# Kernel optimization log

Hardware: AMD Instinct MI355X
Metric: run time of the kernel (lower is better)

The kernel has to match this reference:

```python
import jax, jax.numpy as jnp
import numpy as np

NUM_HEADS = 4
GROUPS = 16
EPS = 1e-5


def setup_inputs() -> dict:
    key = jax.random.key(0)
    ks = jax.random.split(key, 7)
    b, c, hh, ww = 4, 256, 64, 64
    x = jax.random.normal(ks[0], (b, c, hh, ww), dtype=jnp.float32)
    norm_w = 1.0 + 0.1 * jax.random.normal(ks[1], (c,), dtype=jnp.float32)
    norm_b = 0.1 * jax.random.normal(ks[2], (c,), dtype=jnp.float32)
    qkv_w = jax.random.normal(ks[3], (3 * c, c), dtype=jnp.float32) / np.sqrt(c)
    qkv_b = 0.01 * jax.random.normal(ks[4], (3 * c,), dtype=jnp.float32)
    # NOTE: original zero-inits proj_out; we use random weights so the
    # attention path actually affects the output (kernel correctness test).
    proj_w = jax.random.normal(ks[5], (c, c), dtype=jnp.float32) / np.sqrt(c)
    proj_b = jnp.zeros((c,), dtype=jnp.float32)
    return {"x": x, "norm_w": norm_w, "norm_b": norm_b,
            "qkv_w": qkv_w, "qkv_b": qkv_b,
            "proj_w": proj_w, "proj_b": proj_b}


def _group_norm(x, w, b):
    # x: [B, C, T]; GroupNorm32 computes in fp32 (inputs already fp32)
    B, C, T = x.shape
    xg = x.reshape(B, GROUPS, C // GROUPS, T)
    mean = jnp.mean(xg, axis=(2, 3), keepdims=True)
    var = jnp.var(xg, axis=(2, 3), keepdims=True)
    xn = ((xg - mean) * jax.lax.rsqrt(var + EPS)).reshape(B, C, T)
    return xn * w[None, :, None] + b[None, :, None]


def reference(x, norm_w, norm_b, qkv_w, qkv_b, proj_w, proj_b):
    b, c = x.shape[0], x.shape[1]
    spatial = x.shape[2:]
    x2 = x.reshape(b, c, -1)                       # [B, C, T]
    T = x2.shape[-1]
    normed = _group_norm(x2, norm_w, norm_b)
    qkv = jnp.einsum('oc,bct->bot', qkv_w, normed) + qkv_b[None, :, None]
    # faithful reshape: [B, 3C, T] -> [B*H, 3C/H, T], then split in thirds
    qkv = qkv.reshape(b * NUM_HEADS, (3 * c) // NUM_HEADS, T)
    ch = qkv.shape[1] // 3                         # = C / H
    q, k, v = jnp.split(qkv, 3, axis=1)
    scale = 1.0 / np.sqrt(np.sqrt(ch))
    weight = jnp.einsum('bct,bcs->bts', q * scale, k * scale)
    weight = jax.nn.softmax(weight.astype(jnp.float32), axis=-1).astype(qkv.dtype)
    h = jnp.einsum('bts,bcs->bct', weight, v)      # [B*H, ch, T]
    h = h.reshape(b, c, T)
    h = jnp.einsum('oc,bct->bot', proj_w, h) + proj_b[None, :, None]
    return (x2 + h).reshape(b, c, *spatial)
```

## Files before the change

### kernel.cpp

```cpp
#include <hip/hip_runtime.h>

constexpr int kB  = 4;
constexpr int kC  = 256;
constexpr int kT  = 4096;
constexpr int kG  = 16;
constexpr int kCg = kC / kG;
constexpr int kH  = 4;
constexpr int kCh = kC / kH;
constexpr float kEps = 1e-5f;
constexpr float kQScale = 0.125f * 1.4426950408889634f;

typedef short bf16x8 __attribute__((ext_vector_type(8)));
typedef float f32x4  __attribute__((ext_vector_type(4)));
typedef float f32x16 __attribute__((ext_vector_type(16)));

__device__ inline unsigned short f2bf(float f) {
    union { float f; unsigned u; } v; v.f = f;
    unsigned r = v.u + 0x7fffu + ((v.u >> 16) & 1u);
    return (unsigned short)(r >> 16);
}
__device__ inline unsigned pk2bf(float a, float b) {
    return (unsigned)f2bf(a) | ((unsigned)f2bf(b) << 16);
}
__device__ inline unsigned pk2bf_trunc(float a, float b) {
    return __builtin_amdgcn_perm(__float_as_uint(b), __float_as_uint(a), 0x07060302u);
}

__global__ __launch_bounds__(256) void gn_stats_kernel(const float* __restrict__ x,
                                                       float* __restrict__ stats) {
    int bg = blockIdx.x;
    const float4* xp4 = (const float4*)(x + (size_t)bg * (kCg * kT));
    int tid = threadIdx.x;
    float s = 0.f, q = 0.f;
    #pragma unroll 4
    for (int i = 0; i < (kCg * kT / 4) / 256; ++i) {
        float4 v = xp4[tid + i * 256];
        s += v.x + v.y + v.z + v.w;
        q += v.x * v.x + v.y * v.y + v.z * v.z + v.w * v.w;
    }
    #pragma unroll
    for (int off = 32; off > 0; off >>= 1) {
        s += __shfl_down(s, off);
        q += __shfl_down(q, off);
    }
    __shared__ float rs[4], rq[4];
    int wid = tid >> 6, lane = tid & 63;
    if (lane == 0) { rs[wid] = s; rq[wid] = q; }
    __syncthreads();
    if (tid == 0) {
        float S = rs[0] + rs[1] + rs[2] + rs[3];
        float Q = rq[0] + rq[1] + rq[2] + rq[3];
        const float invN = 1.0f / (float)(kCg * kT);
        float mean = S * invN;
        float var  = Q * invN - mean * mean;
        stats[bg * 2 + 0] = mean;
        stats[bg * 2 + 1] = rsqrtf(var + kEps);
    }
}

__global__ __launch_bounds__(256) void gn_apply_t_kernel(const float* __restrict__ x,
                                                         const float* __restrict__ stats,
                                                         const float* __restrict__ w,
                                                         const float* __restrict__ bias,
                                                         unsigned short* __restrict__ normT) {
    __shared__ float Ls[64][65];
    int t0 = blockIdx.x * 64;
    int c0 = blockIdx.y * 64;
    int b  = blockIdx.z;
    int tid = threadIdx.x;
    #pragma unroll
    for (int p = 0; p < 4; ++p) {
        int idx = tid + p * 256;
        int cl = idx >> 4, t4 = idx & 15;
        int c = c0 + cl;
        int bg = b * kG + (c >> 4);
        float mean = stats[bg * 2 + 0];
        float rstd = stats[bg * 2 + 1];
        float sw = w[c] * rstd;
        float sb = bias[c] - mean * sw;
        float4 v = *(const float4*)&x[((size_t)b * kC + c) * kT + t0 + t4 * 4];
        Ls[t4 * 4 + 0][cl] = v.x * sw + sb;
        Ls[t4 * 4 + 1][cl] = v.y * sw + sb;
        Ls[t4 * 4 + 2][cl] = v.z * sw + sb;
        Ls[t4 * 4 + 3][cl] = v.w * sw + sb;
    }
    __syncthreads();
    {
        int row = tid >> 2, cq = (tid & 3) * 16;
        unsigned tmp[8];
        #pragma unroll
        for (int i = 0; i < 8; ++i)
            tmp[i] = pk2bf(Ls[row][cq + 2 * i], Ls[row][cq + 2 * i + 1]);
        uint4* dst = (uint4*)&normT[((size_t)b * kT + t0 + row) * kC + c0 + cq];
        dst[0] = make_uint4(tmp[0], tmp[1], tmp[2], tmp[3]);
        dst[1] = make_uint4(tmp[4], tmp[5], tmp[6], tmp[7]);
    }
}

__global__ __launch_bounds__(256) void wcvt_kernel(const float* __restrict__ qkv_w,
                                                   const float* __restrict__ proj_w,
                                                   unsigned short* __restrict__ wbf) {
    int gid = blockIdx.x * 256 + threadIdx.x;
    for (int i = gid; i < 65536; i += gridDim.x * 256) {
        float4 v = (i < 49152) ? ((const float4*)qkv_w)[i]
                               : ((const float4*)proj_w)[i - 49152];
        *(uint2*)&wbf[(size_t)i * 4] = make_uint2(pk2bf(v.x, v.y), pk2bf(v.z, v.w));
    }
}

__global__ __launch_bounds__(256) void qkv_gemm_kernel(const unsigned short* __restrict__ wbf,
                                                       const float* __restrict__ qkv_b,
                                                       const unsigned short* __restrict__ normT,
                                                       unsigned short* __restrict__ qTg,
                                                       unsigned short* __restrict__ kTg,
                                                       unsigned short* __restrict__ vCg) {
    constexpr int LDK = 72;
    constexpr int LDV = 136;
    __shared__ __align__(16) unsigned short As[64 * LDK];
    __shared__ __align__(16) unsigned short Bs[128 * LDK];

    int t0 = blockIdx.x * 128;
    int m0 = blockIdx.y * 64;
    int b  = blockIdx.z;
    const unsigned short* Ab = wbf + (size_t)m0 * kC;
    const unsigned short* Bb = normT + (size_t)b * kT * kC;

    int tid = threadIdx.x;
    int wave = tid >> 6, lane = tid & 63;
    int ln15 = lane & 15, quad = lane >> 4;
    int wm = wave >> 1, wt = wave & 1;

    f32x4 acc[2][4] = {};

    for (int k0 = 0; k0 < kC; k0 += 64) {
        __syncthreads();
        #pragma unroll
        for (int p = 0; p < 2; ++p) {
            int idx = tid + p * 256;
            int row = idx >> 3, seg = idx & 7;
            *(uint4*)&As[row * LDK + seg * 8] =
                *(const uint4*)&Ab[(size_t)row * kC + k0 + seg * 8];
        }
        #pragma unroll
        for (int p = 0; p < 4; ++p) {
            int idx = tid + p * 256;
            int row = idx >> 3, seg = idx & 7;
            *(uint4*)&Bs[row * LDK + seg * 8] =
                *(const uint4*)&Bb[(size_t)(t0 + row) * kC + k0 + seg * 8];
        }
        __syncthreads();
        #pragma unroll
        for (int ks = 0; ks < 2; ++ks) {
            bf16x8 af[2], bf[4];
            #pragma unroll
            for (int i = 0; i < 2; ++i)
                af[i] = *(bf16x8*)&As[(wm * 32 + i * 16 + ln15) * LDK + ks * 32 + quad * 8];
            #pragma unroll
            for (int j = 0; j < 4; ++j)
                bf[j] = *(bf16x8*)&Bs[(wt * 64 + j * 16 + ln15) * LDK + ks * 32 + quad * 8];
            #pragma unroll
            for (int i = 0; i < 2; ++i)
                #pragma unroll
                for (int j = 0; j < 4; ++j)
                    acc[i][j] = __builtin_amdgcn_mfma_f32_16x16x32_bf16(
                        af[i], bf[j], acc[i][j], 0, 0, 0);
        }
    }

    int type = (m0 % 192) / 64;
    int h = m0 / 192;
    int bh = b * kH + h;
    __syncthreads();
    #pragma unroll
    for (int i = 0; i < 2; ++i) {
        float4 bv = *(const float4*)&qkv_b[m0 + wm * 32 + i * 16 + quad * 4];
        const float* bp = (const float*)&bv;
        #pragma unroll
        for (int j = 0; j < 4; ++j) {
            int tl = wt * 64 + j * 16 + ln15;
            int c = wm * 32 + i * 16 + quad * 4;
            float v0 = acc[i][j][0] + bp[0];
            float v1 = acc[i][j][1] + bp[1];
            float v2 = acc[i][j][2] + bp[2];
            float v3 = acc[i][j][3] + bp[3];
            if (type == 0) {
                v0 *= kQScale; v1 *= kQScale; v2 *= kQScale; v3 *= kQScale;
            }
            if (type != 2) {
                *(uint2*)&Bs[tl * LDK + c] = make_uint2(pk2bf(v0, v1), pk2bf(v2, v3));
            } else {
                Bs[(c + 0) * LDV + tl] = f2bf(v0);
                Bs[(c + 1) * LDV + tl] = f2bf(v1);
                Bs[(c + 2) * LDV + tl] = f2bf(v2);
                Bs[(c + 3) * LDV + tl] = f2bf(v3);
            }
        }
    }
    __syncthreads();
    if (type != 2) {
        unsigned short* base = ((type == 0) ? qTg : kTg) + (size_t)bh * (kT * kCh);
        #pragma unroll
        for (int p = 0; p < 4; ++p) {
            int f = tid + p * 256;
            int ln = f & 31, hif = (f >> 5) & 1, ks = (f >> 6) & 3, tb = f >> 8;
            *(uint4*)&base[((t0 >> 5) + tb) * 2048 + ks * 512 + hif * 256 + ln * 8] =
                *(uint4*)&Bs[(tb * 32 + ln) * LDK + ks * 16 + hif * 8];
        }
    } else {
        unsigned short* base = vCg + (size_t)bh * (kT * kCh);
        #pragma unroll
        for (int p = 0; p < 4; ++p) {
            int f = tid + p * 256;
            int c = f & 63, hif = (f >> 6) & 1, sg = f >> 7;
            *(uint4*)&base[((t0 >> 4) + sg) * 1024 + hif * 512 + c * 8] =
                *(uint4*)&Bs[c * LDV + sg * 16 + hif * 8];
        }
    }
}

__global__ __launch_bounds__(256, 4) void attn_mfma_kernel(const unsigned short* __restrict__ qTg,
                                                           const unsigned short* __restrict__ kTg,
                                                           const unsigned short* __restrict__ vCg,
                                                           unsigned short* __restrict__ attnT) {
    constexpr int LDK = 72;
    __shared__ __align__(16) unsigned short Ps[64 * LDK];
    __shared__ float l_part[2][64];

    int bh = blockIdx.y;
    int t0 = blockIdx.x * 64;
    int b = bh >> 2, h = bh & 3;

    int tid = threadIdx.x;
    int wave = tid >> 6, lane = tid & 63;
    int ln31 = lane & 31, hi = lane >> 5;
    int sh = wave >> 1, th = wave & 1;

    const unsigned short* qb = qTg + (size_t)bh * (kT * kCh);
    const unsigned short* kb = kTg + (size_t)bh * (kT * kCh);
    const unsigned short* vb = vCg + (size_t)bh * (kT * kCh);

    bf16x8 qf[4];
    {
        const unsigned short* qp = qb + ((t0 >> 5) + th) * 2048 + hi * 256 + ln31 * 8;
        #pragma unroll
        for (int ks = 0; ks < 4; ++ks) qf[ks] = *(const bf16x8*)(qp + ks * 512);
    }
    const unsigned short* kptr = kb + sh * 2048 + hi * 256 + ln31 * 8;
    const unsigned short* vptr = vb + hi * 512 + (sh * 32 + ln31) * 8;

    bf16x8 kf[4], vf[4];
    #pragma unroll
    for (int ks = 0; ks < 4; ++ks) kf[ks] = *(const bf16x8*)(kptr + ks * 512);
    #pragma unroll
    for (int ks = 0; ks < 4; ++ks) vf[ks] = *(const bf16x8*)(vptr + ks * 1024);

    float l_r = 0.f;
    f32x16 accO = {};

    for (int s0 = 0; s0 < kT; s0 += 64) {
        f32x16 accS = {};
        #pragma unroll
        for (int ks = 0; ks < 4; ++ks)
            accS = __builtin_amdgcn_mfma_f32_32x32x16_bf16(kf[ks], qf[ks], accS, 0, 0, 0);

        if (s0 + 64 < kT) {
            kptr += 4096;
            #pragma unroll
            for (int ks = 0; ks < 4; ++ks) kf[ks] = *(const bf16x8*)(kptr + ks * 512);
        }

        int t = th * 32 + ln31;
        float rs = 0.f;
        #pragma unroll
        for (int g = 0; g < 4; ++g) {
            float p0 = __builtin_amdgcn_exp2f(accS[4 * g + 0]);
            float p1 = __builtin_amdgcn_exp2f(accS[4 * g + 1]);
            float p2 = __builtin_amdgcn_exp2f(accS[4 * g + 2]);
            float p3 = __builtin_amdgcn_exp2f(accS[4 * g + 3]);
            rs += (p0 + p1) + (p2 + p3);
            *(uint2*)&Ps[t * LDK + sh * 32 + 8 * g + 4 * hi] =
                make_uint2(pk2bf_trunc(p0, p1), pk2bf_trunc(p2, p3));
        }
        rs += __shfl_xor(rs, 32);
        l_r += rs;
        __syncthreads();

        #pragma unroll
        for (int ks = 0; ks < 4; ++ks) {
            bf16x8 pf = *(bf16x8*)&Ps[(th * 32 + ln31) * LDK + ks * 16 + hi * 8];
            accO = __builtin_amdgcn_mfma_f32_32x32x16_bf16(vf[ks], pf, accO, 0, 0, 0);
        }

        if (s0 + 64 < kT) {
            vptr += 4096;
            #pragma unroll
            for (int ks = 0; ks < 4; ++ks) vf[ks] = *(const bf16x8*)(vptr + ks * 1024);
        }
        __syncthreads();
    }

    if (hi == 0) l_part[sh][th * 32 + ln31] = l_r;
    __syncthreads();
    int t = th * 32 + ln31;
    float linv = 1.0f / (l_part[0][t] + l_part[1][t]);
    #pragma unroll
    for (int g = 0; g < 4; ++g) {
        int c = sh * 32 + 8 * g + 4 * hi;
        float v0 = accO[4 * g + 0] * linv;
        float v1 = accO[4 * g + 1] * linv;
        float v2 = accO[4 * g + 2] * linv;
        float v3 = accO[4 * g + 3] * linv;
        *(uint2*)&attnT[((size_t)b * kT + t0 + t) * kC + h * kCh + c] =
            make_uint2(pk2bf(v0, v1), pk2bf(v2, v3));
    }
}

__global__ __launch_bounds__(256) void proj_gemm_kernel(const unsigned short* __restrict__ wpbf,
                                                        const float* __restrict__ proj_b,
                                                        const unsigned short* __restrict__ attnT,
                                                        const float* __restrict__ x,
                                                        float* __restrict__ out) {
    constexpr int LDK = 72;
    __shared__ __align__(16) unsigned short As[64 * LDK];
    __shared__ __align__(16) unsigned short Bs[128 * LDK];

    int t0 = blockIdx.x * 128;
    int m0 = blockIdx.y * 64;
    int b  = blockIdx.z;
    const unsigned short* Ab = wpbf + (size_t)m0 * kC;
    const unsigned short* Bb = attnT + (size_t)b * kT * kC;

    int tid = threadIdx.x;
    int wave = tid >> 6, lane = tid & 63;
    int ln15 = lane & 15, quad = lane >> 4;
    int wm = wave >> 1, wt = wave & 1;

    f32x4 acc[2][4] = {};

    for (int k0 = 0; k0 < kC; k0 += 64) {
        __syncthreads();
        #pragma unroll
        for (int p = 0; p < 2; ++p) {
            int idx = tid + p * 256;
            int row = idx >> 3, seg = idx & 7;
            *(uint4*)&As[row * LDK + seg * 8] =
                *(const uint4*)&Ab[(size_t)row * kC + k0 + seg * 8];
        }
        #pragma unroll
        for (int p = 0; p < 4; ++p) {
            int idx = tid + p * 256;
            int row = idx >> 3, seg = idx & 7;
            *(uint4*)&Bs[row * LDK + seg * 8] =
                *(const uint4*)&Bb[(size_t)(t0 + row) * kC + k0 + seg * 8];
        }
        __syncthreads();
        #pragma unroll
        for (int ks = 0; ks < 2; ++ks) {
            bf16x8 af[2], bf[4];
            #pragma unroll
            for (int i = 0; i < 2; ++i)
                af[i] = *(bf16x8*)&As[(wm * 32 + i * 16 + ln15) * LDK + ks * 32 + quad * 8];
            #pragma unroll
            for (int j = 0; j < 4; ++j)
                bf[j] = *(bf16x8*)&Bs[(wt * 64 + j * 16 + ln15) * LDK + ks * 32 + quad * 8];
            #pragma unroll
            for (int i = 0; i < 2; ++i)
                #pragma unroll
                for (int j = 0; j < 4; ++j)
                    acc[i][j] = __builtin_amdgcn_mfma_f32_16x16x32_bf16(
                        af[i], bf[j], acc[i][j], 0, 0, 0);
        }
    }

    #pragma unroll
    for (int i = 0; i < 2; ++i) {
        float4 bv = *(const float4*)&proj_b[m0 + wm * 32 + i * 16 + quad * 4];
        const float* bp = (const float*)&bv;
        #pragma unroll
        for (int j = 0; j < 4; ++j) {
            int t = t0 + wt * 64 + j * 16 + ln15;
            int mbase = m0 + wm * 32 + i * 16 + quad * 4;
            #pragma unroll
            for (int r = 0; r < 4; ++r) {
                size_t off = ((size_t)b * kC + mbase + r) * kT + t;
                out[off] = acc[i][j][r] + bp[r] + x[off];
            }
        }
    }
}

extern "C" void kernel_launch(void* const* d_in, const int* in_sizes, int n_in,
                              void* d_out, int out_size, void* d_ws, size_t ws_size,
                              hipStream_t stream) {
    const float* x      = (const float*)d_in[0];
    const float* norm_w = (const float*)d_in[1];
    const float* norm_b = (const float*)d_in[2];
    const float* qkv_w  = (const float*)d_in[3];
    const float* qkv_b  = (const float*)d_in[4];
    const float* proj_w = (const float*)d_in[5];
    const float* proj_b = (const float*)d_in[6];
    float* out = (float*)d_out;

    float* stats = (float*)d_ws;
    unsigned short* wsbf  = (unsigned short*)((float*)d_ws + 128);
    unsigned short* normT = wsbf;
    unsigned short* wbf   = normT + (size_t)kB * kT * kC;
    unsigned short* qTp   = wbf + 262144;
    unsigned short* kTp   = qTp + (size_t)kB * kH * kT * kCh;
    unsigned short* vCp   = kTp + (size_t)kB * kH * kT * kCh;
    unsigned short* attnT = vCp + (size_t)kB * kH * kT * kCh;
    unsigned short* wpbf  = wbf + 196608;

    gn_stats_kernel<<<kB * kG, 256, 0, stream>>>(x, stats);
    gn_apply_t_kernel<<<dim3(kT / 64, kC / 64, kB), 256, 0, stream>>>(
        x, stats, norm_w, norm_b, normT);
    wcvt_kernel<<<128, 256, 0, stream>>>(qkv_w, proj_w, wbf);
    qkv_gemm_kernel<<<dim3(kT / 128, 12, kB), 256, 0, stream>>>(
        wbf, qkv_b, normT, qTp, kTp, vCp);
    attn_mfma_kernel<<<dim3(kT / 64, kB * kH), 256, 0, stream>>>(qTp, kTp, vCp, attnT);
    proj_gemm_kernel<<<dim3(kT / 128, kC / 64, kB), 256, 0, stream>>>(
        wpbf, proj_b, attnT, x, out);
}
```

Before: 218.5 us.

## Give each attention wave full key blocks with private P tiles, drop block syncs

The attention kernel now processes 128 query rows per block, one 32-row slab per wave. Each wave covers all 64 keys and all 64 value channels itself, so the P tile lives in a per-wave LDS slice and the two __syncthreads per key step and the cross-wave row-sum reduction go away. The cost is doubled K/V register fragments per wave, a lower occupancy bound (launch_bounds 2), and a grid half as large. Separately, the weight conversion kernel is merged into the group-norm stats kernel to save one launch.

```diff
diff --git a/kernel.cpp b/kernel.cpp
--- a/kernel.cpp
+++ b/kernel.cpp
@@ -26,11 +26,23 @@
     return __builtin_amdgcn_perm(__float_as_uint(b), __float_as_uint(a), 0x07060302u);
 }
 
-__global__ __launch_bounds__(256) void gn_stats_kernel(const float* __restrict__ x,
-                                                       float* __restrict__ stats) {
+__global__ __launch_bounds__(256) void prep_kernel(const float* __restrict__ x,
+                                                   float* __restrict__ stats,
+                                                   const float* __restrict__ qkv_w,
+                                                   const float* __restrict__ proj_w,
+                                                   unsigned short* __restrict__ wbf) {
+    int tid = threadIdx.x;
+    if (blockIdx.x >= 64) {
+        int gid = (blockIdx.x - 64) * 256 + tid;
+        for (int i = gid; i < 65536; i += 128 * 256) {
+            float4 v = (i < 49152) ? ((const float4*)qkv_w)[i]
+                                   : ((const float4*)proj_w)[i - 49152];
+            *(uint2*)&wbf[(size_t)i * 4] = make_uint2(pk2bf(v.x, v.y), pk2bf(v.z, v.w));
+        }
+        return;
+    }
     int bg = blockIdx.x;
     const float4* xp4 = (const float4*)(x + (size_t)bg * (kCg * kT));
-    int tid = threadIdx.x;
     float s = 0.f, q = 0.f;
     #pragma unroll 4
     for (int i = 0; i < (kCg * kT / 4) / 256; ++i) {
@@ -94,17 +106,6 @@
         uint4* dst = (uint4*)&normT[((size_t)b * kT + t0 + row) * kC + c0 + cq];
         dst[0] = make_uint4(tmp[0], tmp[1], tmp[2], tmp[3]);
         dst[1] = make_uint4(tmp[4], tmp[5], tmp[6], tmp[7]);
-    }
-}
-
-__global__ __launch_bounds__(256) void wcvt_kernel(const float* __restrict__ qkv_w,
-                                                   const float* __restrict__ proj_w,
-                                                   unsigned short* __restrict__ wbf) {
-    int gid = blockIdx.x * 256 + threadIdx.x;
-    for (int i = gid; i < 65536; i += gridDim.x * 256) {
-        float4 v = (i < 49152) ? ((const float4*)qkv_w)[i]
-                               : ((const float4*)proj_w)[i - 49152];
-        *(uint2*)&wbf[(size_t)i * 4] = make_uint2(pk2bf(v.x, v.y), pk2bf(v.z, v.w));
     }
 }
 
@@ -218,22 +219,21 @@
     }
 }
 
-__global__ __launch_bounds__(256, 4) void attn_mfma_kernel(const unsigned short* __restrict__ qTg,
+__global__ __launch_bounds__(256, 2) void attn_mfma_kernel(const unsigned short* __restrict__ qTg,
                                                            const unsigned short* __restrict__ kTg,
                                                            const unsigned short* __restrict__ vCg,
                                                            unsigned short* __restrict__ attnT) {
-    constexpr int LDK = 72;
-    __shared__ __align__(16) unsigned short Ps[64 * LDK];
-    __shared__ float l_part[2][64];
+    constexpr int LDPu = 36;
+    __shared__ __align__(16) unsigned int Ps[4][32 * LDPu];
 
     int bh = blockIdx.y;
-    int t0 = blockIdx.x * 64;
+    int t0 = blockIdx.x * 128;
     int b = bh >> 2, h = bh & 3;
 
     int tid = threadIdx.x;
     int wave = tid >> 6, lane = tid & 63;
     int ln31 = lane & 31, hi = lane >> 5;
-    int sh = wave >> 1, th = wave & 1;
+    unsigned int* Pw = &Ps[wave][0];
 
     const unsigned short* qb = qTg + (size_t)bh * (kT * kCh);
     const unsigned short* kb = kTg + (size_t)bh * (kT * kCh);
@@ -241,77 +241,100 @@
 
     bf16x8 qf[4];
     {
-        const unsigned short* qp = qb + ((t0 >> 5) + th) * 2048 + hi * 256 + ln31 * 8;
+        const unsigned short* qp = qb + ((t0 >> 5) + wave) * 2048 + hi * 256 + ln31 * 8;
         #pragma unroll
         for (int ks = 0; ks < 4; ++ks) qf[ks] = *(const bf16x8*)(qp + ks * 512);
     }
-    const unsigned short* kptr = kb + sh * 2048 + hi * 256 + ln31 * 8;
-    const unsigned short* vptr = vb + hi * 512 + (sh * 32 + ln31) * 8;
-
-    bf16x8 kf[4], vf[4];
-    #pragma unroll
-    for (int ks = 0; ks < 4; ++ks) kf[ks] = *(const bf16x8*)(kptr + ks * 512);
-    #pragma unroll
-    for (int ks = 0; ks < 4; ++ks) vf[ks] = *(const bf16x8*)(vptr + ks * 1024);
+    const unsigned short* kptr = kb + hi * 256 + ln31 * 8;
+    const unsigned short* vptr = vb + hi * 512 + ln31 * 8;
+
+    bf16x8 kf[8], vf[8];
+    #pragma unroll
+    for (int i = 0; i < 8; ++i)
+        kf[i] = *(const bf16x8*)(kptr + (i >> 2) * 2048 + (i & 3) * 512);
+    #pragma unroll
+    for (int i = 0; i < 8; ++i)
+        vf[i] = *(const bf16x8*)(vptr + (i & 3) * 1024 + (i >> 2) * 256);
 
     float l_r = 0.f;
-    f32x16 accO = {};
+    f32x16 accO0 = {}, accO1 = {};
+    union PunP { uint4 u; bf16x8 f; };
 
     for (int s0 = 0; s0 < kT; s0 += 64) {
-        f32x16 accS = {};
+        f32x16 accS0 = {}, accS1 = {};
         #pragma unroll
         for (int ks = 0; ks < 4; ++ks)
-            accS = __builtin_amdgcn_mfma_f32_32x32x16_bf16(kf[ks], qf[ks], accS, 0, 0, 0);
+            accS0 = __builtin_amdgcn_mfma_f32_32x32x16_bf16(kf[ks], qf[ks], accS0, 0, 0, 0);
+        #pragma unroll
+        for (int ks = 0; ks < 4; ++ks)
+            accS1 = __builtin_amdgcn_mfma_f32_32x32x16_bf16(kf[4 + ks], qf[ks], accS1, 0, 0, 0);
 
         if (s0 + 64 < kT) {
             kptr += 4096;
             #pragma unroll
-            for (int ks = 0; ks < 4; ++ks) kf[ks] = *(const bf16x8*)(kptr + ks * 512);
-        }
-
-        int t = th * 32 + ln31;
+            for (int i = 0; i < 8; ++i)
+                kf[i] = *(const bf16x8*)(kptr + (i >> 2) * 2048 + (i & 3) * 512);
+        }
+
         float rs = 0.f;
         #pragma unroll
         for (int g = 0; g < 4; ++g) {
-            float p0 = __builtin_amdgcn_exp2f(accS[4 * g + 0]);
-            float p1 = __builtin_amdgcn_exp2f(accS[4 * g + 1]);
-            float p2 = __builtin_amdgcn_exp2f(accS[4 * g + 2]);
-            float p3 = __builtin_amdgcn_exp2f(accS[4 * g + 3]);
+            float p0 = __builtin_amdgcn_exp2f(accS0[4 * g + 0]);
+            float p1 = __builtin_amdgcn_exp2f(accS0[4 * g + 1]);
+            float p2 = __builtin_amdgcn_exp2f(accS0[4 * g + 2]);
+            float p3 = __builtin_amdgcn_exp2f(accS0[4 * g + 3]);
             rs += (p0 + p1) + (p2 + p3);
-            *(uint2*)&Ps[t * LDK + sh * 32 + 8 * g + 4 * hi] =
-                make_uint2(pk2bf_trunc(p0, p1), pk2bf_trunc(p2, p3));
+            int ui = ln31 * LDPu + 4 * g + 2 * hi;
+            Pw[ui + 0] = pk2bf_trunc(p0, p1);
+            Pw[ui + 1] = pk2bf_trunc(p2, p3);
+        }
+        #pragma unroll
+        for (int g = 0; g < 4; ++g) {
+            float p0 = __builtin_amdgcn_exp2f(accS1[4 * g + 0]);
+            float p1 = __builtin_amdgcn_exp2f(accS1[4 * g + 1]);
+            float p2 = __builtin_amdgcn_exp2f(accS1[4 * g + 2]);
+            float p3 = __builtin_amdgcn_exp2f(accS1[4 * g + 3]);
+            rs += (p0 + p1) + (p2 + p3);
+            int ui = ln31 * LDPu + 16 + 4 * g + 2 * hi;
+            Pw[ui + 0] = pk2bf_trunc(p0, p1);
+            Pw[ui + 1] = pk2bf_trunc(p2, p3);
         }
         rs += __shfl_xor(rs, 32);
         l_r += rs;
-        __syncthreads();
-
-        #pragma unroll
-        for (int ks = 0; ks < 4; ++ks) {
-            bf16x8 pf = *(bf16x8*)&Ps[(th * 32 + ln31) * LDK + ks * 16 + hi * 8];
-            accO = __builtin_amdgcn_mfma_f32_32x32x16_bf16(vf[ks], pf, accO, 0, 0, 0);
+        __asm__ __volatile__("" ::: "memory");
+
+        #pragma unroll
+        for (int i = 0; i < 4; ++i) {
+            PunP pk;
+            pk.u = *(const uint4*)&Pw[ln31 * LDPu + i * 8 + hi * 4];
+            accO0 = __builtin_amdgcn_mfma_f32_32x32x16_bf16(vf[i],     pk.f, accO0, 0, 0, 0);
+            accO1 = __builtin_amdgcn_mfma_f32_32x32x16_bf16(vf[4 + i], pk.f, accO1, 0, 0, 0);
         }
 
         if (s0 + 64 < kT) {
             vptr += 4096;
             #pragma unroll
-            for (int ks = 0; ks < 4; ++ks) vf[ks] = *(const bf16x8*)(vptr + ks * 1024);
-        }
-        __syncthreads();
-    }
-
-    if (hi == 0) l_part[sh][th * 32 + ln31] = l_r;
-    __syncthreads();
-    int t = th * 32 + ln31;
-    float linv = 1.0f / (l_part[0][t] + l_part[1][t]);
-    #pragma unroll
-    for (int g = 0; g < 4; ++g) {
-        int c = sh * 32 + 8 * g + 4 * hi;
-        float v0 = accO[4 * g + 0] * linv;
-        float v1 = accO[4 * g + 1] * linv;
-        float v2 = accO[4 * g + 2] * linv;
-        float v3 = accO[4 * g + 3] * linv;
-        *(uint2*)&attnT[((size_t)b * kT + t0 + t) * kC + h * kCh + c] =
-            make_uint2(pk2bf(v0, v1), pk2bf(v2, v3));
+            for (int i = 0; i < 8; ++i)
+                vf[i] = *(const bf16x8*)(vptr + (i & 3) * 1024 + (i >> 2) * 256);
+        }
+        __asm__ __volatile__("" ::: "memory");
+    }
+
+    float linv = 1.0f / l_r;
+    int t = t0 + wave * 32 + ln31;
+    #pragma unroll
+    for (int ct = 0; ct < 2; ++ct) {
+        const f32x16& ao = ct ? accO1 : accO0;
+        #pragma unroll
+        for (int g = 0; g < 4; ++g) {
+            int c = h * kCh + ct * 32 + 8 * g + 4 * hi;
+            float v0 = ao[4 * g + 0] * linv;
+            float v1 = ao[4 * g + 1] * linv;
+            float v2 = ao[4 * g + 2] * linv;
+            float v3 = ao[4 * g + 3] * linv;
+            *(uint2*)&attnT[((size_t)b * kT + t) * kC + c] =
+                make_uint2(pk2bf(v0, v1), pk2bf(v2, v3));
+        }
     }
 }
 
@@ -411,13 +434,12 @@
     unsigned short* attnT = vCp + (size_t)kB * kH * kT * kCh;
     unsigned short* wpbf  = wbf + 196608;
 
-    gn_stats_kernel<<<kB * kG, 256, 0, stream>>>(x, stats);
+    prep_kernel<<<192, 256, 0, stream>>>(x, stats, qkv_w, proj_w, wbf);
     gn_apply_t_kernel<<<dim3(kT / 64, kC / 64, kB), 256, 0, stream>>>(
         x, stats, norm_w, norm_b, normT);
-    wcvt_kernel<<<128, 256, 0, stream>>>(qkv_w, proj_w, wbf);
     qkv_gemm_kernel<<<dim3(kT / 128, 12, kB), 256, 0, stream>>>(
         wbf, qkv_b, normT, qTp, kTp, vCp);
-    attn_mfma_kernel<<<dim3(kT / 64, kB * kH), 256, 0, stream>>>(qTp, kTp, vCp, attnT);
+    attn_mfma_kernel<<<dim3(kT / 128, kB * kH), 256, 0, stream>>>(qTp, kTp, vCp, attnT);
     proj_gemm_kernel<<<dim3(kT / 128, kC / 64, kB), 256, 0, stream>>>(
         wpbf, proj_b, attnT, x, out);
 }
```

Result: no change. 215.7 us (-1.3%).
